# Optimization experiments

Hardware: AMD Instinct MI355X
Metric: run time of the kernel (lower is better)

Reference implementation:

```python
import jax, jax.numpy as jnp
import numpy as np

B, S, F, H = 256, 512, 64, 128
ODE_STEPS = 4
MAX_DT = 1.0


def setup_inputs() -> dict:
    key = jax.random.key(0)
    ks = jax.random.split(key, 11)
    D = F + H  # concat(x_t, h) width
    xav = float(np.sqrt(6.0 / (D + H)))          # xavier_uniform for gate weights
    bsc = float(1.0 / np.sqrt(D))                # torch Linear default bias init
    x = jax.random.normal(ks[0], (B, S, F), jnp.float32)
    time_diffs = jax.random.uniform(ks[1], (B, S), jnp.float32, 0.1, 2.0)
    def w(k):
        return jax.random.uniform(k, (D, H), jnp.float32, -xav, xav)
    def b(k):
        return jax.random.uniform(k, (H,), jnp.float32, -bsc, bsc)
    return {
        "x": x, "time_diffs": time_diffs,
        "W_i": w(ks[2]), "b_i": b(ks[3]),
        "W_f": w(ks[4]), "b_f": b(ks[5]),
        "W_o": w(ks[6]), "b_o": b(ks[7]),
        "W_g": w(ks[8]), "b_g": b(ks[9]),
    }


def reference(x, time_diffs, W_i, b_i, W_f, b_f, W_o, b_o, W_g, b_g):
    def ode_func(x_t, h, c):
        comb = jnp.concatenate([x_t, h], axis=-1)  # [B, F+H]
        i = jax.nn.sigmoid(comb @ W_i + b_i)
        f = jax.nn.sigmoid(comb @ W_f + b_f)
        o = jax.nn.sigmoid(comb @ W_o + b_o)
        g = jnp.tanh(comb @ W_g + b_g)
        dc = i * g + f * c - c
        dh = o * jnp.tanh(c) - h
        return dh, dc

    def rk4_step(x_t, h, c, dt):  # dt: [B, 1]
        k1h, k1c = ode_func(x_t, h, c)
        k2h, k2c = ode_func(x_t, h + 0.5 * dt * k1h, c + 0.5 * dt * k1c)
        k3h, k3c = ode_func(x_t, h + 0.5 * dt * k2h, c + 0.5 * dt * k2c)
        k4h, k4c = ode_func(x_t, h + dt * k3h, c + dt * k3c)
        h_new = h + dt / 6.0 * (k1h + 2 * k2h + 2 * k3h + k4h)
        c_new = c + dt / 6.0 * (k1c + 2 * k2c + 2 * k3c + k4c)
        return h_new, c_new

    def time_step(carry, inp):
        h, c = carry
        x_t, dtv = inp  # x_t [B,F], dtv [B]
        sub_dt = (jnp.minimum(dtv, MAX_DT) / ODE_STEPS)[:, None]  # [B,1]
        def body(hc, _):
            hh, cc = hc
            return rk4_step(x_t, hh, cc, sub_dt), None
        (h, c), _ = jax.lax.scan(body, (h, c), None, length=ODE_STEPS)
        return (h, c), h

    h0 = jnp.zeros((x.shape[0], H), x.dtype)
    c0 = jnp.zeros((x.shape[0], H), x.dtype)
    xs = (jnp.swapaxes(x, 0, 1), jnp.swapaxes(time_diffs, 0, 1))  # [S,B,F], [S,B]
    _, hs = jax.lax.scan(time_step, (h0, c0), xs)  # [S,B,H]
    return jnp.swapaxes(hs, 0, 1)  # [B,S,H]
```

## Files before the change

### kernel.cpp

```cpp
#include <hip/hip_runtime.h>


#define B_N 256
#define S_N 512
#define F_N 64
#define H_N 128

typedef _Float16 v8h __attribute__((ext_vector_type(8)));
typedef float v4f __attribute__((ext_vector_type(4)));

static __device__ __forceinline__ float sigm(float x) {
  float e = __builtin_amdgcn_exp2f(-1.442695040888963f * x);
  return __builtin_amdgcn_rcpf(1.0f + e);
}

__global__ void __launch_bounds__(512, 2) clstm_mfma(
    const float* __restrict__ x,
    const float* __restrict__ td,
    const float* __restrict__ Wi, const float* __restrict__ bi,
    const float* __restrict__ Wf, const float* __restrict__ bff,
    const float* __restrict__ Wo, const float* __restrict__ bo,
    const float* __restrict__ Wg, const float* __restrict__ bg,
    float* __restrict__ out)
{
  const int b    = blockIdx.x;
  const int t    = threadIdx.x;
  const int wv   = t >> 6;
  const int l    = t & 63;
  const int col  = l & 15;
  const int quad = l >> 4;
  const int n    = wv * 16 + col;

  const float* Wptr[4] = {Wi, Wf, Wo, Wg};
  v8h Bw[4][6];
#pragma unroll
  for (int g = 0; g < 4; ++g) {
    const float* W = Wptr[g];
#pragma unroll
    for (int kt = 0; kt < 6; ++kt) {
      v8h f;
#pragma unroll
      for (int j = 0; j < 8; ++j)
        f[j] = (_Float16)W[(kt * 32 + quad * 8 + j) * H_N + n];
      Bw[g][kt] = f;
    }
  }
  v4f cb[4];
#pragma unroll
  for (int g = 0; g < 4; ++g) {
    float bv = (g == 0 ? bi : g == 1 ? bff : g == 2 ? bo : bg)[n];
    cb[g][0] = bv; cb[g][1] = bv; cb[g][2] = bv; cb[g][3] = bv;
  }

  __shared__ alignas(16) _Float16 lds_h[2][H_N];
  __shared__ alignas(16) _Float16 lds_x[F_N];
  __shared__ float lds_td[S_N];

  lds_td[t] = (t < S_N) ? td[b * S_N + t] : 0.f;
  if (t < 32) {
    const float* xr = x + (size_t)b * S_N * F_N;
    lds_x[2 * t]     = (_Float16)xr[2 * t];
    lds_x[2 * t + 1] = (_Float16)xr[2 * t + 1];
  }
  if (t < H_N) lds_h[0][t] = (_Float16)0.0f;
  __syncthreads();

  float h0v = 0.f, c0v = 0.f;
  float h_ev = 0.f, c_ev = 0.f;
  float sum_h = 0.f, sum_c = 0.f;
  const v4f zf = {0.f, 0.f, 0.f, 0.f};

  for (int s = 0; s < S_N; ++s) {
    float dt  = fminf(lds_td[s], 1.0f) * 0.25f;
    float hdt = 0.5f * dt;
    float d6  = dt * (1.0f / 6.0f);

    v8h ax0 = *(const v8h*)(lds_x + quad * 8);
    v8h ax1 = *(const v8h*)(lds_x + 32 + quad * 8);
    v4f xpD[4];
#pragma unroll
    for (int g = 0; g < 4; ++g) {
      v4f a = __builtin_amdgcn_mfma_f32_16x16x32_f16(ax0, Bw[g][0], cb[g], 0, 0, 0);
      xpD[g] = __builtin_amdgcn_mfma_f32_16x16x32_f16(ax1, Bw[g][1], a, 0, 0, 0);
    }

    float xn0 = 0.f, xn1 = 0.f;
    if (t < 32 && s + 1 < S_N) {
      const float* xr = x + (size_t)(b * S_N + s + 1) * F_N;
      xn0 = xr[2 * t]; xn1 = xr[2 * t + 1];
    }

#pragma unroll 1
    for (int ode = 0; ode < 4; ++ode) {
#pragma unroll
      for (int st = 0; st < 4; ++st) {
        const _Float16* hb = lds_h[st & 1];
        v8h ah0 = *(const v8h*)(hb + quad * 8);
        v8h ah1 = *(const v8h*)(hb + 32 + quad * 8);
        v8h ah2 = *(const v8h*)(hb + 64 + quad * 8);
        v8h ah3 = *(const v8h*)(hb + 96 + quad * 8);
        float pre[4];
#pragma unroll
        for (int g = 0; g < 4; ++g) {
          v4f d0 = __builtin_amdgcn_mfma_f32_16x16x32_f16(ah0, Bw[g][2], xpD[g], 0, 0, 0);
          d0 = __builtin_amdgcn_mfma_f32_16x16x32_f16(ah1, Bw[g][3], d0, 0, 0, 0);
          v4f d1 = __builtin_amdgcn_mfma_f32_16x16x32_f16(ah2, Bw[g][4], zf, 0, 0, 0);
          d1 = __builtin_amdgcn_mfma_f32_16x16x32_f16(ah3, Bw[g][5], d1, 0, 0, 0);
          pre[g] = d0[0] + d1[0];
        }
        float ai = sigm(pre[0]);
        float af = sigm(pre[1]);
        float ao = sigm(pre[2]);
        float ag = fmaf(2.0f, sigm(2.0f * pre[3]), -1.0f);
        float tc = fmaf(2.0f, sigm(2.0f * c_ev), -1.0f);
        float kc = fmaf(ai, ag, (af - 1.0f) * c_ev);
        float kh = fmaf(ao, tc, -h_ev);

        float h_nx, c_nx;
        if (st == 0) {
          sum_h = kh; sum_c = kc;
          h_nx = fmaf(hdt, kh, h0v); c_nx = fmaf(hdt, kc, c0v);
        } else if (st == 1) {
          sum_h = fmaf(2.f, kh, sum_h); sum_c = fmaf(2.f, kc, sum_c);
          h_nx = fmaf(hdt, kh, h0v); c_nx = fmaf(hdt, kc, c0v);
        } else if (st == 2) {
          sum_h = fmaf(2.f, kh, sum_h); sum_c = fmaf(2.f, kc, sum_c);
          h_nx = fmaf(dt, kh, h0v); c_nx = fmaf(dt, kc, c0v);
        } else {
          sum_h += kh; sum_c += kc;
          h0v = fmaf(d6, sum_h, h0v); c0v = fmaf(d6, sum_c, c0v);
          h_nx = h0v; c_nx = c0v;
        }

        if (quad == 0) lds_h[(st & 1) ^ 1][n] = (_Float16)h_nx;
        if (st == 3 && ode == 3 && t < 32 && s + 1 < S_N) {
          lds_x[2 * t]     = (_Float16)xn0;
          lds_x[2 * t + 1] = (_Float16)xn1;
        }
        __syncthreads();
        h_ev = h_nx; c_ev = c_nx;
      }
    }

    if (quad == 0) out[(size_t)(b * S_N + s) * H_N + n] = h0v;
  }
}

extern "C" void kernel_launch(void* const* d_in, const int* in_sizes, int n_in,
                              void* d_out, int out_size, void* d_ws, size_t ws_size,
                              hipStream_t stream) {
  (void)in_sizes; (void)n_in; (void)d_ws; (void)ws_size; (void)out_size;
  clstm_mfma<<<B_N, 512, 0, stream>>>(
      (const float*)d_in[0],
      (const float*)d_in[1],
      (const float*)d_in[2], (const float*)d_in[3],
      (const float*)d_in[4], (const float*)d_in[5],
      (const float*)d_in[6], (const float*)d_in[7],
      (const float*)d_in[8], (const float*)d_in[9],
      (float*)d_out);
}
```

Baseline: 3.790 ms.

## Move input-weight fragments to LDS and split recurrent MFMA chains into independent accumulators

Keeps the x-projection weight fragments (first 64 rows) in shared memory instead of registers, so fewer VGPRs are held across the recurrence. The per-gate hidden-state MFMAs become four independent MFMAs summed at the end instead of two dependent chains of two, shortening the serial MFMA dependency on the critical path. This costs extra LDS traffic once per timestep and 64KB of shared memory per block, which may limit how many blocks fit per CU.

```diff
diff --git a/kernel.cpp b/kernel.cpp
--- a/kernel.cpp
+++ b/kernel.cpp
@@ -14,7 +14,7 @@
   return __builtin_amdgcn_rcpf(1.0f + e);
 }
 
-__global__ void __launch_bounds__(512, 2) clstm_mfma(
+__global__ void __launch_bounds__(512, 2) clstm_mfma2(
     const float* __restrict__ x,
     const float* __restrict__ td,
     const float* __restrict__ Wi, const float* __restrict__ bi,
@@ -32,17 +32,18 @@
   const int n    = wv * 16 + col;
 
   const float* Wptr[4] = {Wi, Wf, Wo, Wg};
-  v8h Bw[4][6];
+
+  v8h Bh[4][4];
 #pragma unroll
   for (int g = 0; g < 4; ++g) {
     const float* W = Wptr[g];
 #pragma unroll
-    for (int kt = 0; kt < 6; ++kt) {
+    for (int kt = 0; kt < 4; ++kt) {
       v8h f;
 #pragma unroll
       for (int j = 0; j < 8; ++j)
-        f[j] = (_Float16)W[(kt * 32 + quad * 8 + j) * H_N + n];
-      Bw[g][kt] = f;
+        f[j] = (_Float16)W[(64 + kt * 32 + quad * 8 + j) * H_N + n];
+      Bh[g][kt] = f;
     }
   }
   v4f cb[4];
@@ -52,11 +53,24 @@
     cb[g][0] = bv; cb[g][1] = bv; cb[g][2] = bv; cb[g][3] = bv;
   }
 
+  __shared__ alignas(16) v8h lds_wx[8][512];
   __shared__ alignas(16) _Float16 lds_h[2][H_N];
   __shared__ alignas(16) _Float16 lds_x[F_N];
   __shared__ float lds_td[S_N];
 
-  lds_td[t] = (t < S_N) ? td[b * S_N + t] : 0.f;
+#pragma unroll
+  for (int g = 0; g < 4; ++g) {
+    const float* W = Wptr[g];
+#pragma unroll
+    for (int kt = 0; kt < 2; ++kt) {
+      v8h f;
+#pragma unroll
+      for (int j = 0; j < 8; ++j)
+        f[j] = (_Float16)W[(kt * 32 + quad * 8 + j) * H_N + n];
+      lds_wx[g * 2 + kt][t] = f;
+    }
+  }
+  lds_td[t] = td[b * S_N + t];
   if (t < 32) {
     const float* xr = x + (size_t)b * S_N * F_N;
     lds_x[2 * t]     = (_Float16)xr[2 * t];
@@ -80,8 +94,10 @@
     v4f xpD[4];
 #pragma unroll
     for (int g = 0; g < 4; ++g) {
-      v4f a = __builtin_amdgcn_mfma_f32_16x16x32_f16(ax0, Bw[g][0], cb[g], 0, 0, 0);
-      xpD[g] = __builtin_amdgcn_mfma_f32_16x16x32_f16(ax1, Bw[g][1], a, 0, 0, 0);
+      v8h b0 = lds_wx[g * 2 + 0][t];
+      v8h b1 = lds_wx[g * 2 + 1][t];
+      v4f a = __builtin_amdgcn_mfma_f32_16x16x32_f16(ax0, b0, cb[g], 0, 0, 0);
+      xpD[g] = __builtin_amdgcn_mfma_f32_16x16x32_f16(ax1, b1, a, 0, 0, 0);
     }
 
     float xn0 = 0.f, xn1 = 0.f;
@@ -102,11 +118,11 @@
         float pre[4];
 #pragma unroll
         for (int g = 0; g < 4; ++g) {
-          v4f d0 = __builtin_amdgcn_mfma_f32_16x16x32_f16(ah0, Bw[g][2], xpD[g], 0, 0, 0);
-          d0 = __builtin_amdgcn_mfma_f32_16x16x32_f16(ah1, Bw[g][3], d0, 0, 0, 0);
-          v4f d1 = __builtin_amdgcn_mfma_f32_16x16x32_f16(ah2, Bw[g][4], zf, 0, 0, 0);
-          d1 = __builtin_amdgcn_mfma_f32_16x16x32_f16(ah3, Bw[g][5], d1, 0, 0, 0);
-          pre[g] = d0[0] + d1[0];
+          v4f d0 = __builtin_amdgcn_mfma_f32_16x16x32_f16(ah0, Bh[g][0], xpD[g], 0, 0, 0);
+          v4f d1 = __builtin_amdgcn_mfma_f32_16x16x32_f16(ah1, Bh[g][1], zf, 0, 0, 0);
+          v4f d2 = __builtin_amdgcn_mfma_f32_16x16x32_f16(ah2, Bh[g][2], zf, 0, 0, 0);
+          v4f d3 = __builtin_amdgcn_mfma_f32_16x16x32_f16(ah3, Bh[g][3], zf, 0, 0, 0);
+          pre[g] = (d0[0] + d1[0]) + (d2[0] + d3[0]);
         }
         float ai = sigm(pre[0]);
         float af = sigm(pre[1]);
@@ -150,7 +166,7 @@
                               void* d_out, int out_size, void* d_ws, size_t ws_size,
                               hipStream_t stream) {
   (void)in_sizes; (void)n_in; (void)d_ws; (void)ws_size; (void)out_size;
-  clstm_mfma<<<B_N, 512, 0, stream>>>(
+  clstm_mfma2<<<B_N, 512, 0, stream>>>(
       (const float*)d_in[0],
       (const float*)d_in[1],
       (const float*)d_in[2], (const float*)d_in[3],
```

After: 4.199 ms. 1.11x slower.
